# Kernel optimization log

Measured on AMD Instinct MI355X. Metric: run time of the kernel, lower is better.

Reference implementation:

```python
import jax, jax.numpy as jnp
import numpy as np
import math

N_HEAD = 16
STRIDE = 128
C = 8


def _sparse_causal_mask(q_len, k_len):
    # Mirrors LingLongAttention._sparse_causal_mask (static, host-side numpy).
    cols = np.arange(k_len)
    rows = np.arange(k_len)[:, None]
    strided = (cols % STRIDE) >= (STRIDE - C)          # last C cols of each stride block
    local = (cols[None, :] // STRIDE) == (rows // STRIDE)  # same stride block as query
    causal = cols[None, :] <= rows
    layout = (strided[None, :] | local) & causal       # [k_len, k_len]
    return jnp.asarray(layout[k_len - q_len:])         # [q_len, k_len]


def setup_inputs() -> dict:
    key = jax.random.key(0)
    k1, k2, k3 = jax.random.split(key, 3)
    B, S, E = 2, 2048, 1024
    return {
        "hidden_states": jax.random.normal(k1, (B, S, E), dtype=jnp.float32),
        "W_attn": jax.random.normal(k2, (E, 3 * E), dtype=jnp.float32) * 0.02,
        "b_attn": jnp.zeros((3 * E,), dtype=jnp.float32),
        "W_proj": jax.random.normal(k3, (E, E), dtype=jnp.float32) * 0.02,
        "b_proj": jnp.zeros((E,), dtype=jnp.float32),
    }


def reference(hidden_states, W_attn, b_attn, W_proj, b_proj):
    B, S, E = hidden_states.shape
    H = N_HEAD
    D = E // H
    # Conv1D: x @ W + b, then split into q,k,v
    qkv = hidden_states @ W_attn + b_attn                 # [B,S,3E]
    q, k, v = jnp.split(qkv, 3, axis=-1)
    split = lambda t: t.reshape(B, S, H, D).transpose(0, 2, 1, 3)  # [B,H,S,D]
    q, k, v = split(q), split(k), split(v)
    scale = jnp.asarray(1.0 / math.sqrt(D), dtype=q.dtype)
    scores = jnp.einsum("bhqd,bhkd->bhqk", q, k) * scale  # [B,H,S,S]
    mask = _sparse_causal_mask(S, S)[None, None]          # [1,1,S,S]
    mask_value = jnp.asarray(jnp.finfo(scores.dtype).min, dtype=scores.dtype)
    scores = jnp.where(mask, scores, mask_value)
    attn = jax.nn.softmax(scores, axis=-1)
    out = jnp.einsum("bhqk,bhkd->bhqd", attn, v)          # [B,H,S,D]
    out = out.transpose(0, 2, 1, 3).reshape(B, S, E)      # merge heads
    return out @ W_proj + b_proj
```

## Files before the change

kernel.cpp:

```cpp
#include <hip/hip_runtime.h>
#include <hip/hip_bf16.h>
#include <stdint.h>

typedef unsigned short u16;
typedef uint32_t u32;
typedef short s16x8 __attribute__((ext_vector_type(8)));
typedef float f32x4 __attribute__((ext_vector_type(4)));

#define SDIM 2048
#define EDIM 1024

static __device__ __forceinline__ float b2f(u16 v) {
    union { float f; u32 u; } c; c.u = ((u32)v) << 16; return c.f;
}
static __device__ __forceinline__ u16 f2b(float f) {
    union { float f; u32 u; } c; c.f = f;
    u32 u = c.u;
    u32 r = (u + 0x7FFFu + ((u >> 16) & 1u)) >> 16;
    return (u16)r;
}
static __device__ __forceinline__ void gll16(const u16* g, u16* l) {
    __builtin_amdgcn_global_load_lds(
        (const __attribute__((address_space(1))) void*)g,
        (__attribute__((address_space(3))) void*)l, 16, 0, 0);
}

static __device__ __forceinline__ int sniff_bf16(const u16* __restrict__ x) {
    u16 v = x[(threadIdx.x & 63) * 2];
    int e = (v >> 7) & 0xFF;
    unsigned long long m = __ballot(e >= 90 && e <= 144);
    return __popcll(m) >= 48;
}

__global__ __launch_bounds__(256) void k_prep(
    const void* __restrict__ X, const void* __restrict__ Wa,
    const void* __restrict__ Wp, u16* __restrict__ Xb,
    u16* __restrict__ WtA, u16* __restrict__ WtP) {
    int f = sniff_bf16((const u16*)X);
    int z = blockIdx.z;
    int t = threadIdx.x;
    if (z == 2) {
        if (f) return;
        const float* s = (const float*)X;
        int bid = blockIdx.y * 48 + blockIdx.x;
        for (int c = bid; c < 2048; c += 768) {
            long i = ((long)c * 256 + t) * 8;
            u16 o[8];
            for (int j = 0; j < 8; ++j) o[j] = f2b(s[i + j]);
            *(uint4*)&Xb[i] = *(uint4*)o;
        }
        return;
    }
    if (z == 1 && blockIdx.x >= 16) return;
    const void* src = z ? Wp : Wa;
    u16* dst = z ? WtP : WtA;
    int Nsrc = z ? 1024 : 3072;
    int n0 = blockIdx.x * 64, k0 = blockIdx.y * 64;
    __shared__ u16 L[64 * 72];
    int r = t >> 2, c0 = (t & 3) * 16;
    u16 val[16];
    if (f) {
        const u16* s = (const u16*)src + (size_t)(k0 + r) * Nsrc + n0 + c0;
        *(uint4*)&val[0] = *(const uint4*)s;
        *(uint4*)&val[8] = *(const uint4*)(s + 8);
    } else {
        const float* s = (const float*)src + (size_t)(k0 + r) * Nsrc + n0 + c0;
        for (int j = 0; j < 16; ++j) val[j] = f2b(s[j]);
    }
    for (int j = 0; j < 16; ++j) L[(c0 + j) * 72 + r] = val[j];
    __syncthreads();
    uint4 o0 = *(const uint4*)&L[r * 72 + c0];
    uint4 o1 = *(const uint4*)&L[r * 72 + c0 + 8];
    u16* d = dst + (size_t)(n0 + r) * 1024 + k0 + c0;
    *(uint4*)d = o0;
    *(uint4*)(d + 8) = o1;
}

#define STA6(s, Tn) gll16(Asrc + (size_t)(s) * 64 * 1024 + ((Tn) & 15) * 64, \
                          &As[(Tn) & 1][(((s) * 64) + wave * 8) * 64])
#define STB6(s, Tn) gll16(Bsrc + (size_t)(s) * 64 * 1024 + ((Tn) & 15) * 64, \
                          &Bs[(Tn) & 1][(((s) * 64) + wave * 8) * 64])

__global__ __launch_bounds__(512, 2) void k_gemm1(
    const u16* __restrict__ Xraw, const u16* __restrict__ Xb,
    const u16* __restrict__ Bt, const void* __restrict__ bias,
    u16* __restrict__ C) {
    const int K = 1024;
    __shared__ u16 As[2][256 * 64];
    __shared__ u16 Bs[2][192 * 64];
    int f = sniff_bf16(Xraw);
    const u16* A = f ? Xraw : Xb;
    int t = threadIdx.x, wave = t >> 6, lane = t & 63;
    int bid = blockIdx.x;
    int swz = (bid & 7) * 32 + (bid >> 3);
    int bx = swz & 15, by = swz >> 4;
    int m0 = by * 256, n0 = bx * 192;
    int wr = wave >> 2, wc = wave & 3;
    int lm = lane & 15, q4 = lane >> 4;
    int l8 = lane >> 3, l7 = lane & 7;
    int scol = (l7 ^ l8) * 8;
    const u16* Asrc = A  + (size_t)(m0 + wave * 8 + l8) * K + scol;
    const u16* Bsrc = Bt + (size_t)(n0 + wave * 8 + l8) * K + scol;
    int kc0 = (q4 ^ (lm & 7)) * 8;
    int kc1 = ((4 + q4) ^ (lm & 7)) * 8;

    f32x4 acc[8][3];
    f32x4 z = {0.f, 0.f, 0.f, 0.f};
#pragma unroll
    for (int mi = 0; mi < 8; ++mi)
#pragma unroll
        for (int ni = 0; ni < 3; ++ni) acc[mi][ni] = z;

    STA6(0, 0); STA6(1, 0); STA6(2, 0); STA6(3, 0);
    STB6(0, 0); STB6(1, 0); STB6(2, 0);
    STA6(0, 1); STA6(1, 1); STA6(2, 1); STA6(3, 1);

    s16x8 afr[8][2], bfr[3][2];

    for (int T = 0; T < 16; ++T) {
        int p = T & 1;
        asm volatile("s_waitcnt vmcnt(4)\n\ts_barrier" ::: "memory");
#pragma unroll
        for (int mi = 0; mi < 4; ++mi) {
            int rb = (wr * 128 + mi * 16 + lm) * 64;
            afr[mi][0] = *(const s16x8*)&As[p][rb + kc0];
            afr[mi][1] = *(const s16x8*)&As[p][rb + kc1];
        }
#pragma unroll
        for (int ni = 0; ni < 2; ++ni) {
            int rb = (wc * 48 + ni * 16 + lm) * 64;
            bfr[ni][0] = *(const s16x8*)&Bs[p][rb + kc0];
            bfr[ni][1] = *(const s16x8*)&Bs[p][rb + kc1];
        }
        STB6(0, T + 1);
        __builtin_amdgcn_s_setprio(1);
#pragma unroll
        for (int mi = 0; mi < 4; ++mi)
#pragma unroll
            for (int ni = 0; ni < 2; ++ni) {
                acc[mi][ni] = __builtin_amdgcn_mfma_f32_16x16x32_bf16(
                    afr[mi][0], bfr[ni][0], acc[mi][ni], 0, 0, 0);
                acc[mi][ni] = __builtin_amdgcn_mfma_f32_16x16x32_bf16(
                    afr[mi][1], bfr[ni][1], acc[mi][ni], 0, 0, 0);
            }
        __builtin_amdgcn_s_setprio(0);
        asm volatile("s_barrier" ::: "memory");
#pragma unroll
        for (int mi = 4; mi < 8; ++mi) {
            int rb = (wr * 128 + mi * 16 + lm) * 64;
            afr[mi][0] = *(const s16x8*)&As[p][rb + kc0];
            afr[mi][1] = *(const s16x8*)&As[p][rb + kc1];
        }
        {
            int rb = (wc * 48 + 32 + lm) * 64;
            bfr[2][0] = *(const s16x8*)&Bs[p][rb + kc0];
            bfr[2][1] = *(const s16x8*)&Bs[p][rb + kc1];
        }
        STB6(1, T + 1); STB6(2, T + 1);
        __builtin_amdgcn_s_setprio(1);
#pragma unroll
        for (int mi = 4; mi < 8; ++mi) {
            acc[mi][2] = __builtin_amdgcn_mfma_f32_16x16x32_bf16(
                afr[mi][0], bfr[2][0], acc[mi][2], 0, 0, 0);
            acc[mi][2] = __builtin_amdgcn_mfma_f32_16x16x32_bf16(
                afr[mi][1], bfr[2][1], acc[mi][2], 0, 0, 0);
        }
        __builtin_amdgcn_s_setprio(0);
        asm volatile("s_barrier" ::: "memory");
        STA6(0, T + 2); STA6(1, T + 2);
        __builtin_amdgcn_s_setprio(1);
#pragma unroll
        for (int mi = 0; mi < 4; ++mi) {
            acc[mi][2] = __builtin_amdgcn_mfma_f32_16x16x32_bf16(
                afr[mi][0], bfr[2][0], acc[mi][2], 0, 0, 0);
            acc[mi][2] = __builtin_amdgcn_mfma_f32_16x16x32_bf16(
                afr[mi][1], bfr[2][1], acc[mi][2], 0, 0, 0);
        }
        __builtin_amdgcn_s_setprio(0);
        asm volatile("s_barrier" ::: "memory");
        STA6(2, T + 2); STA6(3, T + 2);
        __builtin_amdgcn_s_setprio(1);
#pragma unroll
        for (int mi = 4; mi < 8; ++mi)
#pragma unroll
            for (int ni = 0; ni < 2; ++ni) {
                acc[mi][ni] = __builtin_amdgcn_mfma_f32_16x16x32_bf16(
                    afr[mi][0], bfr[ni][0], acc[mi][ni], 0, 0, 0);
                acc[mi][ni] = __builtin_amdgcn_mfma_f32_16x16x32_bf16(
                    afr[mi][1], bfr[ni][1], acc[mi][ni], 0, 0, 0);
            }
        __builtin_amdgcn_s_setprio(0);
        asm volatile("s_barrier" ::: "memory");
    }
    asm volatile("s_waitcnt vmcnt(0)" ::: "memory");

    int cn = lm, cr = q4 * 4;
    float bb[3]; int hm_[3], d_[3];
#pragma unroll
    for (int ni = 0; ni < 3; ++ni) {
        int gn = n0 + wc * 48 + ni * 16 + cn;
        bb[ni] = f ? b2f(((const u16*)bias)[gn]) : ((const float*)bias)[gn];
        int kind = gn >> 10, rem = gn & 1023;
        hm_[ni] = kind * 32 + (rem >> 6);
        d_[ni] = rem & 63;
    }
#pragma unroll
    for (int mi = 0; mi < 8; ++mi)
        for (int r = 0; r < 4; ++r) {
            int gm = m0 + wr * 128 + mi * 16 + cr + r;
            int b = gm >> 11, s = gm & 2047;
#pragma unroll
            for (int ni = 0; ni < 3; ++ni) {
                size_t o = ((size_t)((hm_[ni] + b * 16) * 2048 + s)) * 64 + d_[ni];
                C[o] = f2b(acc[mi][ni][r] + bb[ni]);
            }
        }
}

__global__ __launch_bounds__(256) void k_gemm2(
    const u16* __restrict__ Xraw, const u16* __restrict__ A,
    const u16* __restrict__ Bt, const void* __restrict__ bias,
    u16* __restrict__ Cb, float* __restrict__ Cf) {
    const int K = 1024, N = 1024;
    __shared__ u16 As[3][2048];
    __shared__ u16 Bs[3][4096];
    int f = sniff_bf16(Xraw);
    int t = threadIdx.x, wave = t >> 6, lane = t & 63;
    int m0 = blockIdx.y * 64, n0 = blockIdx.x * 128;
    int wm = (wave >> 1) * 32, wn = (wave & 1) * 64;
    int lm = lane & 15;
    int lk = (((lane >> 4) ^ ((lane >> 1) & 3))) * 8;
    int sr = t >> 2;
    int sc = ((t & 3) ^ ((t >> 3) & 3)) * 8;
    const u16* Ap = A + (size_t)(m0 + sr) * K + sc;
    const u16* Bp = Bt + (size_t)(n0 + sr) * K + sc;
    int wo = wave * 512;

    f32x4 acc[2][4];
    f32x4 z = {0.f, 0.f, 0.f, 0.f};
    for (int mi = 0; mi < 2; ++mi)
        for (int ni = 0; ni < 4; ++ni) acc[mi][ni] = z;

    gll16(Ap, &As[0][wo]);
    gll16(Bp, &Bs[0][wo]);
    gll16(Bp + (size_t)64 * K, &Bs[0][wo + 2048]);
    gll16(Ap + 32, &As[1][wo]);
    gll16(Bp + 32, &Bs[1][wo]);
    gll16(Bp + (size_t)64 * K + 32, &Bs[1][wo + 2048]);

    u16 *Ac = &As[0][0], *An = &As[1][0], *At = &As[2][0];
    u16 *Bc = &Bs[0][0], *Bn = &Bs[1][0], *Btg = &Bs[2][0];

    for (int it = 0; it < 32; ++it) {
        asm volatile("s_waitcnt vmcnt(3)\n\ts_barrier" ::: "memory");
        int kn = ((it + 2) & 31) * 32;
        gll16(Ap + kn, At + wo);
        gll16(Bp + kn, Btg + wo);
        gll16(Bp + (size_t)64 * K + kn, Btg + wo + 2048);

        s16x8 af[2], bfr[4];
        for (int mi = 0; mi < 2; ++mi)
            af[mi] = *(const s16x8*)&Ac[(wm + mi * 16 + lm) * 32 + lk];
        for (int ni = 0; ni < 4; ++ni)
            bfr[ni] = *(const s16x8*)&Bc[(wn + ni * 16 + lm) * 32 + lk];
        for (int mi = 0; mi < 2; ++mi)
            for (int ni = 0; ni < 4; ++ni)
                acc[mi][ni] = __builtin_amdgcn_mfma_f32_16x16x32_bf16(
                    af[mi], bfr[ni], acc[mi][ni], 0, 0, 0);

        u16* tp = Ac; Ac = An; An = At; At = tp;
        tp = Bc; Bc = Bn; Bn = Btg; Btg = tp;
    }
    asm volatile("s_waitcnt vmcnt(0)" ::: "memory");

    int store_f32 = (f == 0);
    int cn = lane & 15, cr = (lane >> 4) * 4;
    for (int ni = 0; ni < 4; ++ni) {
        int gn = n0 + wn + ni * 16 + cn;
        float bb = f ? b2f(((const u16*)bias)[gn]) : ((const float*)bias)[gn];
        for (int mi = 0; mi < 2; ++mi)
            for (int r = 0; r < 4; ++r) {
                int gm = m0 + wm + mi * 16 + cr + r;
                float v = acc[mi][ni][r] + bb;
                size_t o = (size_t)gm * N + gn;
                if (store_f32) Cf[o] = v;
                else           Cb[o] = f2b(v);
            }
    }
}

#define VP 264
#define PP 264
__global__ __launch_bounds__(256) void k_attn4(const u16* __restrict__ QKV,
                                               u16* __restrict__ AO) {
    int bx = blockIdx.x, h = blockIdx.y, b = blockIdx.z;
    int qb = bx >> 1, sb = bx & 1;
    int t = threadIdx.x, lane = t & 63, wave = t >> 6;
    int lm = lane & 15, q4 = lane >> 4;
    int nstr = qb << 3;
    int nk = nstr + (sb << 6) + 64;
    int r0 = (qb << 7) + (sb << 6);

    __shared__ char smem[79872];
    u16* Vts = (u16*)smem;
    u16* Qs  = (u16*)(smem + 33792);
    u16* Ks  = (u16*)(smem + 33792 + 9216);
    u16* Ps  = (u16*)(smem + 33792);

    int hm = b * 16 + h;
    const u16* qp = QKV + ((size_t)hm * 2048 + r0) * 64;
    const u16* kp = QKV + ((size_t)(32 + hm) * 2048) * 64;
    const u16* vp = QKV + ((size_t)(64 + hm) * 2048) * 64;

    for (int c = t; c < 512; c += 256) {
        int r = c >> 3, d0 = (c & 7) << 3;
        *(uint4*)&Qs[r * 72 + d0] = *(const uint4*)(qp + c * 8);
    }
    uint4 zz = {0u, 0u, 0u, 0u};
    for (int c = t; c < 2048; c += 256) {
        int i = c >> 3, d0 = (c & 7) << 3;
        uint4 kv = zz;
        if (i < nk) {
            int key = (i < nstr) ? (((i >> 3) << 7) + 120 + (i & 7))
                                 : ((qb << 7) + (i - nstr));
            kv = *(const uint4*)(kp + key * 64 + d0);
        }
        *(uint4*)&Ks[i * 72 + d0] = kv;
    }
    {
        int i0 = (t & 31) * 8, d0 = (t >> 5) * 8;
        u16 m8[8][8];
        for (int r = 0; r < 8; ++r) {
            int i = i0 + r;
            uint4 vv = zz;
            if (i < nk) {
                int key = (i < nstr) ? (((i >> 3) << 7) + 120 + (i & 7))
                                     : ((qb << 7) + (i - nstr));
                vv = *(const uint4*)(vp + key * 64 + d0);
            }
            *(uint4*)m8[r] = vv;
        }
        for (int j = 0; j < 8; ++j) {
            u16 o[8];
            for (int r = 0; r < 8; ++r) o[r] = m8[r][j];
            *(uint4*)&Vts[(d0 + j) * VP + i0] = *(uint4*)o;
        }
    }
    __syncthreads();

    f32x4 acc[16];
    f32x4 z4 = {0.f, 0.f, 0.f, 0.f};
    for (int ni = 0; ni < 16; ++ni) acc[ni] = z4;
    s16x8 af0 = *(const s16x8*)&Qs[(wave * 16 + lm) * 72 + q4 * 8];
    s16x8 af1 = *(const s16x8*)&Qs[(wave * 16 + lm) * 72 + 32 + q4 * 8];
    for (int ni = 0; ni < 16; ++ni) {
        s16x8 bf0 = *(const s16x8*)&Ks[(ni * 16 + lm) * 72 + q4 * 8];
        s16x8 bf1 = *(const s16x8*)&Ks[(ni * 16 + lm) * 72 + 32 + q4 * 8];
        acc[ni] = __builtin_amdgcn_mfma_f32_16x16x32_bf16(af0, bf0, acc[ni], 0, 0, 0);
        acc[ni] = __builtin_amdgcn_mfma_f32_16x16x32_bf16(af1, bf1, acc[ni], 0, 0, 0);
    }
    __syncthreads();

    float mx[4] = {-3e38f, -3e38f, -3e38f, -3e38f};
    for (int ni = 0; ni < 16; ++ni) {
        int i = ni * 16 + lm;
        for (int reg = 0; reg < 4; ++reg) {
            int rl = (sb << 6) + wave * 16 + q4 * 4 + reg;
            bool valid = (i < nstr) || ((i - nstr) <= rl);
            float v = valid ? acc[ni][reg] * 0.125f : -3e38f;
            acc[ni][reg] = v;
            mx[reg] = fmaxf(mx[reg], v);
        }
    }
    for (int reg = 0; reg < 4; ++reg)
        for (int off = 1; off < 16; off <<= 1)
            mx[reg] = fmaxf(mx[reg], __shfl_xor(mx[reg], off, 64));
    float sm[4] = {0.f, 0.f, 0.f, 0.f};
    for (int ni = 0; ni < 16; ++ni)
        for (int reg = 0; reg < 4; ++reg) {
            float e = __expf(acc[ni][reg] - mx[reg]);
            acc[ni][reg] = e;
            sm[reg] += e;
        }
    for (int reg = 0; reg < 4; ++reg)
        for (int off = 1; off < 16; off <<= 1)
            sm[reg] += __shfl_xor(sm[reg], off, 64);
    float inv[4];
    for (int reg = 0; reg < 4; ++reg) inv[reg] = 1.f / sm[reg];

    for (int ni = 0; ni < 16; ++ni) {
        int i = ni * 16 + lm;
        for (int reg = 0; reg < 4; ++reg)
            Ps[(wave * 16 + q4 * 4 + reg) * PP + i] = f2b(acc[ni][reg]);
    }
    __syncthreads();

    f32x4 acc2[4];
    for (int ni2 = 0; ni2 < 4; ++ni2) acc2[ni2] = z4;
    for (int k0 = 0; k0 < 256; k0 += 32) {
        s16x8 pf = *(const s16x8*)&Ps[(wave * 16 + lm) * PP + k0 + q4 * 8];
        for (int ni2 = 0; ni2 < 4; ++ni2) {
            s16x8 vf = *(const s16x8*)&Vts[(ni2 * 16 + lm) * VP + k0 + q4 * 8];
            acc2[ni2] = __builtin_amdgcn_mfma_f32_16x16x32_bf16(pf, vf, acc2[ni2], 0, 0, 0);
        }
    }
    int srow = r0 + wave * 16 + q4 * 4;
    for (int ni2 = 0; ni2 < 4; ++ni2)
        for (int reg = 0; reg < 4; ++reg) {
            size_t o = ((size_t)(b * SDIM + srow + reg)) * EDIM + h * 64 + ni2 * 16 + lm;
            AO[o] = f2b(acc2[ni2][reg] * inv[reg]);
        }
}

extern "C" void kernel_launch(void* const* d_in, const int* in_sizes, int n_in,
                              void* d_out, int out_size, void* d_ws, size_t ws_size,
                              hipStream_t stream) {
    const void* X  = d_in[0];
    const void* Wa = d_in[1];
    const void* ba = d_in[2];
    const void* Wp = d_in[3];
    const void* bp = d_in[4];

    char* w = (char*)d_ws;
    u16* Xb   = (u16*)(w);
    u16* WtA  = (u16*)(w + 8388608);
    u16* WtP  = (u16*)(w + 14680064);
    u16* QKVh = (u16*)(w + 16777216);
    u16* AO   = (u16*)(w + 41943040);

    k_prep<<<dim3(48, 16, 3), 256, 0, stream>>>(X, Wa, Wp, Xb, WtA, WtP);
    k_gemm1<<<dim3(256), 512, 0, stream>>>((const u16*)X, Xb, WtA, ba, QKVh);
    k_attn4<<<dim3(32, 16, 2), 256, 0, stream>>>(QKVh, AO);
    k_gemm2<<<dim3(8, 64), 256, 0, stream>>>((const u16*)X, AO, WtP, bp,
                                             (u16*)d_out, (float*)d_out);
}
```

Measured before the change: 156.9 us.

## Rewrite output projection GEMM with 128x128 tiles and load Q directly to registers

```diff
diff --git a/kernel.cpp b/kernel.cpp
--- a/kernel.cpp
+++ b/kernel.cpp
@@ -217,68 +217,136 @@
         }
 }
 
-__global__ __launch_bounds__(256) void k_gemm2(
+#define STA7(s, Tn) gll16(Asrc + (size_t)(s) * 32 * 1024 + ((Tn) & 15) * 64, \
+                          &As[(Tn) & 1][(((s) * 32) + wave * 8) * 64])
+#define STB7(s, Tn) gll16(Bsrc + (size_t)(s) * 32 * 1024 + ((Tn) & 15) * 64, \
+                          &Bs[(Tn) & 1][(((s) * 32) + wave * 8) * 64])
+
+__global__ __launch_bounds__(256, 2) void k_gemm2(
     const u16* __restrict__ Xraw, const u16* __restrict__ A,
     const u16* __restrict__ Bt, const void* __restrict__ bias,
     u16* __restrict__ Cb, float* __restrict__ Cf) {
     const int K = 1024, N = 1024;
-    __shared__ u16 As[3][2048];
-    __shared__ u16 Bs[3][4096];
+    __shared__ u16 As[2][128 * 64];
+    __shared__ u16 Bs[2][128 * 64];
     int f = sniff_bf16(Xraw);
     int t = threadIdx.x, wave = t >> 6, lane = t & 63;
-    int m0 = blockIdx.y * 64, n0 = blockIdx.x * 128;
-    int wm = (wave >> 1) * 32, wn = (wave & 1) * 64;
-    int lm = lane & 15;
-    int lk = (((lane >> 4) ^ ((lane >> 1) & 3))) * 8;
-    int sr = t >> 2;
-    int sc = ((t & 3) ^ ((t >> 3) & 3)) * 8;
-    const u16* Ap = A + (size_t)(m0 + sr) * K + sc;
-    const u16* Bp = Bt + (size_t)(n0 + sr) * K + sc;
-    int wo = wave * 512;
-
-    f32x4 acc[2][4];
+    int bid = blockIdx.x;
+    int swz = (bid & 7) * 32 + (bid >> 3);
+    int bx = swz & 7, by = swz >> 3;
+    int m0 = by * 128, n0 = bx * 128;
+    int wm = (wave >> 1) * 64, wn = (wave & 1) * 64;
+    int lm = lane & 15, q4 = lane >> 4;
+    int l8 = lane >> 3, l7 = lane & 7;
+    int scol = (l7 ^ l8) * 8;
+    const u16* Asrc = A  + (size_t)(m0 + wave * 8 + l8) * K + scol;
+    const u16* Bsrc = Bt + (size_t)(n0 + wave * 8 + l8) * K + scol;
+    int kc0 = (q4 ^ (lm & 7)) * 8;
+    int kc1 = ((4 + q4) ^ (lm & 7)) * 8;
+
+    f32x4 acc[4][4];
     f32x4 z = {0.f, 0.f, 0.f, 0.f};
-    for (int mi = 0; mi < 2; ++mi)
+#pragma unroll
+    for (int mi = 0; mi < 4; ++mi)
+#pragma unroll
         for (int ni = 0; ni < 4; ++ni) acc[mi][ni] = z;
 
-    gll16(Ap, &As[0][wo]);
-    gll16(Bp, &Bs[0][wo]);
-    gll16(Bp + (size_t)64 * K, &Bs[0][wo + 2048]);
-    gll16(Ap + 32, &As[1][wo]);
-    gll16(Bp + 32, &Bs[1][wo]);
-    gll16(Bp + (size_t)64 * K + 32, &Bs[1][wo + 2048]);
-
-    u16 *Ac = &As[0][0], *An = &As[1][0], *At = &As[2][0];
-    u16 *Bc = &Bs[0][0], *Bn = &Bs[1][0], *Btg = &Bs[2][0];
-
-    for (int it = 0; it < 32; ++it) {
-        asm volatile("s_waitcnt vmcnt(3)\n\ts_barrier" ::: "memory");
-        int kn = ((it + 2) & 31) * 32;
-        gll16(Ap + kn, At + wo);
-        gll16(Bp + kn, Btg + wo);
-        gll16(Bp + (size_t)64 * K + kn, Btg + wo + 2048);
-
-        s16x8 af[2], bfr[4];
+    STA7(0, 0); STA7(1, 0); STA7(2, 0); STA7(3, 0);
+    STB7(0, 0); STB7(1, 0); STB7(2, 0); STB7(3, 0);
+    STA7(0, 1); STA7(1, 1); STA7(2, 1); STA7(3, 1);
+
+    s16x8 afr[4][2], bfr[4][2];
+
+    for (int T = 0; T < 16; ++T) {
+        int p = T & 1;
+        asm volatile("s_waitcnt vmcnt(4)\n\ts_barrier" ::: "memory");
+#pragma unroll
+        for (int mi = 0; mi < 2; ++mi) {
+            int rb = (wm + mi * 16 + lm) * 64;
+            afr[mi][0] = *(const s16x8*)&As[p][rb + kc0];
+            afr[mi][1] = *(const s16x8*)&As[p][rb + kc1];
+        }
+#pragma unroll
+        for (int ni = 0; ni < 2; ++ni) {
+            int rb = (wn + ni * 16 + lm) * 64;
+            bfr[ni][0] = *(const s16x8*)&Bs[p][rb + kc0];
+            bfr[ni][1] = *(const s16x8*)&Bs[p][rb + kc1];
+        }
+        STB7(0, T + 1); STB7(1, T + 1);
+        __builtin_amdgcn_s_setprio(1);
+#pragma unroll
         for (int mi = 0; mi < 2; ++mi)
-            af[mi] = *(const s16x8*)&Ac[(wm + mi * 16 + lm) * 32 + lk];
-        for (int ni = 0; ni < 4; ++ni)
-            bfr[ni] = *(const s16x8*)&Bc[(wn + ni * 16 + lm) * 32 + lk];
+#pragma unroll
+            for (int ni = 0; ni < 2; ++ni) {
+                acc[mi][ni] = __builtin_amdgcn_mfma_f32_16x16x32_bf16(
+                    afr[mi][0], bfr[ni][0], acc[mi][ni], 0, 0, 0);
+                acc[mi][ni] = __builtin_amdgcn_mfma_f32_16x16x32_bf16(
+                    afr[mi][1], bfr[ni][1], acc[mi][ni], 0, 0, 0);
+            }
+        __builtin_amdgcn_s_setprio(0);
+        asm volatile("s_barrier" ::: "memory");
+#pragma unroll
+        for (int mi = 2; mi < 4; ++mi) {
+            int rb = (wm + mi * 16 + lm) * 64;
+            afr[mi][0] = *(const s16x8*)&As[p][rb + kc0];
+            afr[mi][1] = *(const s16x8*)&As[p][rb + kc1];
+        }
+#pragma unroll
+        for (int ni = 2; ni < 4; ++ni) {
+            int rb = (wn + ni * 16 + lm) * 64;
+            bfr[ni][0] = *(const s16x8*)&Bs[p][rb + kc0];
+            bfr[ni][1] = *(const s16x8*)&Bs[p][rb + kc1];
+        }
+        STB7(2, T + 1); STB7(3, T + 1);
+        __builtin_amdgcn_s_setprio(1);
+#pragma unroll
+        for (int mi = 2; mi < 4; ++mi)
+#pragma unroll
+            for (int ni = 2; ni < 4; ++ni) {
+                acc[mi][ni] = __builtin_amdgcn_mfma_f32_16x16x32_bf16(
+                    afr[mi][0], bfr[ni][0], acc[mi][ni], 0, 0, 0);
+                acc[mi][ni] = __builtin_amdgcn_mfma_f32_16x16x32_bf16(
+                    afr[mi][1], bfr[ni][1], acc[mi][ni], 0, 0, 0);
+            }
+        __builtin_amdgcn_s_setprio(0);
+        asm volatile("s_barrier" ::: "memory");
+        STA7(0, T + 2); STA7(1, T + 2);
+        __builtin_amdgcn_s_setprio(1);
+#pragma unroll
         for (int mi = 0; mi < 2; ++mi)
-            for (int ni = 0; ni < 4; ++ni)
-                acc[mi][ni] = __builtin_amdgcn_mfma_f32_16x16x32_bf16(
-                    af[mi], bfr[ni], acc[mi][ni], 0, 0, 0);
-
-        u16* tp = Ac; Ac = An; An = At; At = tp;
-        tp = Bc; Bc = Bn; Bn = Btg; Btg = tp;
+#pragma unroll
+            for (int ni = 2; ni < 4; ++ni) {
+                acc[mi][ni] = __builtin_amdgcn_mfma_f32_16x16x32_bf16(
+                    afr[mi][0], bfr[ni][0], acc[mi][ni], 0, 0, 0);
+                acc[mi][ni] = __builtin_amdgcn_mfma_f32_16x16x32_bf16(
+                    afr[mi][1], bfr[ni][1], acc[mi][ni], 0, 0, 0);
+            }
+        __builtin_amdgcn_s_setprio(0);
+        asm volatile("s_barrier" ::: "memory");
+        STA7(2, T + 2); STA7(3, T + 2);
+        __builtin_amdgcn_s_setprio(1);
+#pragma unroll
+        for (int mi = 2; mi < 4; ++mi)
+#pragma unroll
+            for (int ni = 0; ni < 2; ++ni) {
+                acc[mi][ni] = __builtin_amdgcn_mfma_f32_16x16x32_bf16(
+                    afr[mi][0], bfr[ni][0], acc[mi][ni], 0, 0, 0);
+                acc[mi][ni] = __builtin_amdgcn_mfma_f32_16x16x32_bf16(
+                    afr[mi][1], bfr[ni][1], acc[mi][ni], 0, 0, 0);
+            }
+        __builtin_amdgcn_s_setprio(0);
+        asm volatile("s_barrier" ::: "memory");
     }
     asm volatile("s_waitcnt vmcnt(0)" ::: "memory");
 
     int store_f32 = (f == 0);
     int cn = lane & 15, cr = (lane >> 4) * 4;
+#pragma unroll
     for (int ni = 0; ni < 4; ++ni) {
         int gn = n0 + wn + ni * 16 + cn;
         float bb = f ? b2f(((const u16*)bias)[gn]) : ((const float*)bias)[gn];
-        for (int mi = 0; mi < 2; ++mi)
+#pragma unroll
+        for (int mi = 0; mi < 4; ++mi)
             for (int r = 0; r < 4; ++r) {
                 int gm = m0 + wm + mi * 16 + cr + r;
                 float v = acc[mi][ni][r] + bb;
@@ -301,10 +369,9 @@
     int nk = nstr + (sb << 6) + 64;
     int r0 = (qb << 7) + (sb << 6);
 
-    __shared__ char smem[79872];
+    __shared__ char smem[70656];
     u16* Vts = (u16*)smem;
-    u16* Qs  = (u16*)(smem + 33792);
-    u16* Ks  = (u16*)(smem + 33792 + 9216);
+    u16* Ks  = (u16*)(smem + 33792);
     u16* Ps  = (u16*)(smem + 33792);
 
     int hm = b * 16 + h;
@@ -312,10 +379,10 @@
     const u16* kp = QKV + ((size_t)(32 + hm) * 2048) * 64;
     const u16* vp = QKV + ((size_t)(64 + hm) * 2048) * 64;
 
-    for (int c = t; c < 512; c += 256) {
-        int r = c >> 3, d0 = (c & 7) << 3;
-        *(uint4*)&Qs[r * 72 + d0] = *(const uint4*)(qp + c * 8);
-    }
+    const u16* qrow = qp + (wave * 16 + lm) * 64 + q4 * 8;
+    s16x8 af0 = *(const s16x8*)qrow;
+    s16x8 af1 = *(const s16x8*)(qrow + 32);
+
     uint4 zz = {0u, 0u, 0u, 0u};
     for (int c = t; c < 2048; c += 256) {
         int i = c >> 3, d0 = (c & 7) << 3;
@@ -351,8 +418,6 @@
     f32x4 acc[16];
     f32x4 z4 = {0.f, 0.f, 0.f, 0.f};
     for (int ni = 0; ni < 16; ++ni) acc[ni] = z4;
-    s16x8 af0 = *(const s16x8*)&Qs[(wave * 16 + lm) * 72 + q4 * 8];
-    s16x8 af1 = *(const s16x8*)&Qs[(wave * 16 + lm) * 72 + 32 + q4 * 8];
     for (int ni = 0; ni < 16; ++ni) {
         s16x8 bf0 = *(const s16x8*)&Ks[(ni * 16 + lm) * 72 + q4 * 8];
         s16x8 bf1 = *(const s16x8*)&Ks[(ni * 16 + lm) * 72 + 32 + q4 * 8];
@@ -431,6 +496,6 @@
     k_prep<<<dim3(48, 16, 3), 256, 0, stream>>>(X, Wa, Wp, Xb, WtA, WtP);
     k_gemm1<<<dim3(256), 512, 0, stream>>>((const u16*)X, Xb, WtA, ba, QKVh);
     k_attn4<<<dim3(32, 16, 2), 256, 0, stream>>>(QKVh, AO);
-    k_gemm2<<<dim3(8, 64), 256, 0, stream>>>((const u16*)X, AO, WtP, bp,
-                                             (u16*)d_out, (float*)d_out);
-}
+    k_gemm2<<<dim3(256), 256, 0, stream>>>((const u16*)X, AO, WtP, bp,
+                                           (u16*)d_out, (float*)d_out);
+}
```

Result: slower. 160.5 us (+2.3%).
